# Kernel tuning notes

Measured on AMD Instinct MI355X. Metric: run time of the kernel, lower is better.

The kernel has to match this reference:

```python
import jax, jax.numpy as jnp
import numpy as np

N_U = 100000   # user nodes
N_V = 100000   # item nodes
D = 64         # input_dim
O = 64         # output_dim
R = 5          # num_support (rating levels)
E = 500000     # edges per relation


def setup_inputs() -> dict:
    key = jax.random.key(0)
    ks = jax.random.split(key, 8)
    init_range = np.sqrt(6.0 / (D + O))
    return {
        "x_u": jax.random.normal(ks[0], (N_U, D), jnp.float32),
        "x_v": jax.random.normal(ks[1], (N_V, D), jnp.float32),
        "weights_u": jax.random.uniform(ks[2], (R, D, O), jnp.float32, -init_range, init_range),
        "weights_v": jax.random.uniform(ks[3], (R, D, O), jnp.float32, -init_range, init_range),
        "bias_u": jnp.full((O,), 0.01, jnp.float32),
        "bias_v": jnp.full((O,), 0.01, jnp.float32),
        "edge_val": jax.random.uniform(ks[4], (R, E), jnp.float32),
        "edge_u": jax.random.randint(ks[5], (R, E), 0, N_U, jnp.int32),
        "edge_v": jax.random.randint(ks[6], (R, E), 0, N_V, jnp.int32),
    }


def reference(x_u, x_v, weights_u, weights_v, bias_u, bias_v, edge_val, edge_u, edge_v):
    # Cumulative (ordinal mixture) weights: wu_i = sum_{j<=i} W_u[j]
    Wu = jnp.cumsum(weights_u, axis=0)          # [R, D, O]
    Wv = jnp.cumsum(weights_v, axis=0)          # [R, D, O]

    tmp_u = jnp.einsum("nd,rdo->rno", x_u, Wu)  # [R, N_U, O]
    tmp_v = jnp.einsum("md,rdo->rmo", x_v, Wv)  # [R, N_V, O]

    gather = jax.vmap(lambda t, idx: t[idx])    # per-relation row gather

    # z_u = sum_r support_r @ tmp_v_r : scatter edge messages into user rows
    msg_u = (edge_val[..., None] * gather(tmp_v, edge_v)).reshape(R * E, O)
    z_u = jax.ops.segment_sum(msg_u, edge_u.reshape(-1), num_segments=N_U)

    # z_v = sum_r support_r^T @ tmp_u_r : scatter into item rows
    msg_v = (edge_val[..., None] * gather(tmp_u, edge_u)).reshape(R * E, O)
    z_v = jax.ops.segment_sum(msg_v, edge_v.reshape(-1), num_segments=N_V)

    u_out = jax.nn.relu(z_u + bias_u)
    v_out = jax.nn.relu(z_v + bias_v)
    return (u_out, v_out)
```

## Files before the change

kernel.cpp:

```cpp
#include <hip/hip_runtime.h>

#define N_U 100000
#define N_V 100000
#define OO 64
#define RR 5
#define EE 500000
#define TOT_E (RR * EE)
#define NB 782
#define CAP 4096
#define CAPU 3584
#define SCAT_BLOCKS 306
#define GEMM_BLOCKS 391

typedef short bf16x8 __attribute__((ext_vector_type(8)));
typedef float f32x4 __attribute__((ext_vector_type(4)));

__device__ __forceinline__ float bf2f(unsigned short u) {
  union { unsigned int i; float f; } x;
  x.i = ((unsigned int)u) << 16;
  return x.f;
}
__device__ __forceinline__ unsigned short f2bf(float f) {
  union { float f; unsigned int i; } x;
  x.f = f;
  unsigned int lsb = (x.i >> 16) & 1u;
  unsigned int r = x.i + 0x7fffu + lsb;
  return (unsigned short)(r >> 16);
}

__global__ void prep_weights(const float* __restrict__ wu,
                             const float* __restrict__ wv,
                             unsigned short* __restrict__ bfrag,
                             unsigned* __restrict__ gcur) {
  int side = blockIdx.x;
  if (gcur) {
    unsigned* g = gcur + side * 1024;
    for (int i = threadIdx.x; i < NB; i += 256) g[i] = (unsigned)i * CAP;
  }
  const float* w = side ? wv : wu;
  for (int idx = threadIdx.x; idx < 4096; idx += 256) {
    int d = idx >> 6, o = idx & 63;
    int c = o >> 4, n = o & 15;
    int sk = d >> 5, q = (d >> 3) & 3, jj = d & 7;
    int f = c * 2 + sk;
    int lane = q * 16 + n;
    int pos = (f * 64 + lane) * 8 + jj;
    float acc = 0.f;
    for (int r = 0; r < RR; ++r) {
      acc += w[r * 4096 + idx];
      bfrag[(side * RR + r) * 4096 + pos] = f2bf(acc);
    }
  }
}

__global__ __launch_bounds__(1024) void scatter_gemm(
    const int* __restrict__ dst, const int* __restrict__ src,
    const float* __restrict__ val, unsigned* __restrict__ gcursor,
    unsigned* __restrict__ keyP, unsigned short* __restrict__ valP,
    const float* __restrict__ X,
    const unsigned short* __restrict__ bfrag_side,
    unsigned short* __restrict__ tmp5) {
  __shared__ unsigned lds_u32[18972];
  int blk = blockIdx.x;
  int tid = threadIdx.x;
  if (blk < SCAT_BLOCKS) {
    unsigned* skey = lds_u32;
    unsigned short* sval = (unsigned short*)(lds_u32 + 8192);
    unsigned short* sbid = (unsigned short*)(lds_u32 + 12288);
    unsigned* cnt  = lds_u32 + 16384;
    unsigned* sc   = lds_u32 + 17166;
    unsigned* gbase = lds_u32 + 18190;
    for (int i = tid; i < NB; i += 1024) cnt[i] = 0u;
    __syncthreads();
    int base = blk * 8192;
    int t8 = base + tid * 8;
    bool full = (t8 < TOT_E);
    if (full) {
      int4 d0 = *(const int4*)(dst + t8);
      int4 d1 = *(const int4*)(dst + t8 + 4);
      atomicAdd(&cnt[d0.x >> 7], 1u);
      atomicAdd(&cnt[d0.y >> 7], 1u);
      atomicAdd(&cnt[d0.z >> 7], 1u);
      atomicAdd(&cnt[d0.w >> 7], 1u);
      atomicAdd(&cnt[d1.x >> 7], 1u);
      atomicAdd(&cnt[d1.y >> 7], 1u);
      atomicAdd(&cnt[d1.z >> 7], 1u);
      atomicAdd(&cnt[d1.w >> 7], 1u);
    }
    __syncthreads();
    sc[tid] = (tid < NB) ? cnt[tid] : 0u;
    __syncthreads();
    for (int off = 1; off < 1024; off <<= 1) {
      unsigned a = sc[tid];
      unsigned b = (tid >= off) ? sc[tid - off] : 0u;
      __syncthreads();
      sc[tid] = a + b;
      __syncthreads();
    }
    for (int b = tid; b < NB; b += 1024) {
      unsigned c = cnt[b];
      gbase[b] = c ? atomicAdd(&gcursor[b], c) : 0u;
      cnt[b] = sc[b] - c;
    }
    __syncthreads();
    unsigned total = sc[NB - 1];
    __syncthreads();
    for (int b = tid; b < NB; b += 1024) sc[b] = cnt[b];
    __syncthreads();
    if (full) {
      int4 d0 = *(const int4*)(dst + t8);
      int4 d1 = *(const int4*)(dst + t8 + 4);
      int4 s0 = *(const int4*)(src + t8);
      int4 s1 = *(const int4*)(src + t8 + 4);
      float4 v0 = *(const float4*)(val + t8);
      float4 v1 = *(const float4*)(val + t8 + 4);
      unsigned rb = (unsigned)(t8 / EE) * N_U;
#define PUT(dd, ss, vv)                                                     \
      {                                                                     \
        int bb = (dd) >> 7;                                                 \
        unsigned pos = atomicAdd(&sc[bb], 1u);                              \
        skey[pos] = (((unsigned)((dd) & 127)) << 19) | (rb + (unsigned)(ss)); \
        sval[pos] = f2bf(vv);                                               \
        sbid[pos] = (unsigned short)bb;                                     \
      }
      PUT(d0.x, s0.x, v0.x)
      PUT(d0.y, s0.y, v0.y)
      PUT(d0.z, s0.z, v0.z)
      PUT(d0.w, s0.w, v0.w)
      PUT(d1.x, s1.x, v1.x)
      PUT(d1.y, s1.y, v1.y)
      PUT(d1.z, s1.z, v1.z)
      PUT(d1.w, s1.w, v1.w)
#undef PUT
    }
    __syncthreads();
    for (int i = tid; i < (int)total; i += 1024) {
      unsigned b = sbid[i];
      unsigned addr = gbase[b] + ((unsigned)i - cnt[b]);
      keyP[addr] = skey[i];
      valP[addr] = sval[i];
    }
  } else {
    unsigned short* smem = (unsigned short*)lds_u32;
    for (int i = tid; i < 2560; i += 1024)
      ((bf16x8*)smem)[i] = ((const bf16x8*)bfrag_side)[i];
    __syncthreads();
    int lane = tid & 63;
    int wave = tid >> 6;
    int q = lane >> 4, m = lane & 15;
    int t = (blk - SCAT_BLOCKS) * 16 + wave;
    if (t >= N_U / 16) return;
    int r0 = t * 16;
    const float* xr = X + (size_t)(r0 + m) * 64;
    float4 p0 = *(const float4*)(xr + q * 8);
    float4 p1 = *(const float4*)(xr + q * 8 + 4);
    float4 p2 = *(const float4*)(xr + 32 + q * 8);
    float4 p3 = *(const float4*)(xr + 32 + q * 8 + 4);
    bf16x8 a0, a1;
    a0[0] = (short)f2bf(p0.x); a0[1] = (short)f2bf(p0.y);
    a0[2] = (short)f2bf(p0.z); a0[3] = (short)f2bf(p0.w);
    a0[4] = (short)f2bf(p1.x); a0[5] = (short)f2bf(p1.y);
    a0[6] = (short)f2bf(p1.z); a0[7] = (short)f2bf(p1.w);
    a1[0] = (short)f2bf(p2.x); a1[1] = (short)f2bf(p2.y);
    a1[2] = (short)f2bf(p2.z); a1[3] = (short)f2bf(p2.w);
    a1[4] = (short)f2bf(p3.x); a1[5] = (short)f2bf(p3.y);
    a1[6] = (short)f2bf(p3.z); a1[7] = (short)f2bf(p3.w);
    for (int r = 0; r < RR; ++r) {
      f32x4 acc[4];
#pragma unroll
      for (int c = 0; c < 4; ++c) {
        bf16x8 b0 = *(const bf16x8*)(smem + r * 4096 + ((c * 2 + 0) * 64 + lane) * 8);
        bf16x8 b1 = *(const bf16x8*)(smem + r * 4096 + ((c * 2 + 1) * 64 + lane) * 8);
        f32x4 a = {0.f, 0.f, 0.f, 0.f};
        a = __builtin_amdgcn_mfma_f32_16x16x32_bf16(a0, b0, a, 0, 0, 0);
        a = __builtin_amdgcn_mfma_f32_16x16x32_bf16(a1, b1, a, 0, 0, 0);
        acc[c] = a;
      }
      unsigned short* trow = tmp5 + (size_t)r * N_U * 64;
#pragma unroll
      for (int i = 0; i < 4; ++i) {
        ushort4 o;
        o.x = f2bf(acc[0][i]); o.y = f2bf(acc[1][i]);
        o.z = f2bf(acc[2][i]); o.w = f2bf(acc[3][i]);
        *(ushort4*)(trow + (size_t)(r0 + q * 4 + i) * 64 + m * 4) = o;
      }
    }
  }
}

__global__ __launch_bounds__(512, 8) void bucket_sort_agg(
    const unsigned* __restrict__ keyP, const unsigned short* __restrict__ valP,
    const unsigned* __restrict__ gcursor,
    const unsigned short* __restrict__ tmp5,
    const float* __restrict__ bias, float* __restrict__ out) {
  __shared__ unsigned okey[CAP];
  __shared__ unsigned short oval[CAP];
  __shared__ unsigned hist[128];
  __shared__ unsigned starts[129];
  __shared__ unsigned cur[128];
  int b = blockIdx.x;
  unsigned base = (unsigned)b * CAP;
  int cnt = (int)(gcursor[b] - base);
  if (cnt > CAPU) cnt = CAPU;
  for (int i = threadIdx.x; i < 128; i += 512) hist[i] = 0u;
  __syncthreads();
  for (int i = threadIdx.x; i < cnt; i += 512)
    atomicAdd(&hist[keyP[base + i] >> 19], 1u);
  __syncthreads();
  if (threadIdx.x == 0) {
    unsigned acc = 0u;
    for (int l = 0; l < 128; ++l) {
      starts[l] = acc;
      acc += (hist[l] + 3u) & ~3u;
    }
    starts[128] = acc;
  }
  __syncthreads();
  unsigned tot = starts[128];
  for (int i = threadIdx.x; i < (int)tot; i += 512) { okey[i] = 0u; oval[i] = 0; }
  for (int l = threadIdx.x; l < 128; l += 512) cur[l] = starts[l];
  __syncthreads();
  for (int i = threadIdx.x; i < cnt; i += 512) {
    unsigned k = keyP[base + i];
    unsigned pos = atomicAdd(&cur[k >> 19], 1u);
    okey[pos] = k & 0x7FFFFu;
    oval[pos] = valP[base + i];
  }
  __syncthreads();

  int lane = threadIdx.x & 63;
  int wave = threadIdx.x >> 6;
  int g16 = lane >> 4;
  int m = lane & 15;
  int nb0 = b * 128;
  int nodes = (N_U - nb0 < 128) ? (N_U - nb0) : 128;
  const unsigned short* tp = tmp5 + (m << 2);
  float bl = bias[lane];
  for (int l = wave; l < nodes; l += 8) {
    unsigned s = starts[l];
    unsigned e = starts[l + 1];
    float a0 = 0.f, a1 = 0.f, a2 = 0.f, a3 = 0.f;
    unsigned k = s;
    for (; k + 8 <= e; k += 8) {
      unsigned key0 = okey[k + g16];
      unsigned key1 = okey[k + 4 + g16];
      float v0 = bf2f(oval[k + g16]);
      float v1 = bf2f(oval[k + 4 + g16]);
      ushort4 t0 = *(const ushort4*)(tp + (size_t)key0 * 64);
      ushort4 t1 = *(const ushort4*)(tp + (size_t)key1 * 64);
      a0 += v0 * bf2f(t0.x);
      a1 += v0 * bf2f(t0.y);
      a2 += v0 * bf2f(t0.z);
      a3 += v0 * bf2f(t0.w);
      a0 += v1 * bf2f(t1.x);
      a1 += v1 * bf2f(t1.y);
      a2 += v1 * bf2f(t1.z);
      a3 += v1 * bf2f(t1.w);
    }
    if (k < e) {
      unsigned key0 = okey[k + g16];
      float v0 = bf2f(oval[k + g16]);
      ushort4 t0 = *(const ushort4*)(tp + (size_t)key0 * 64);
      a0 += v0 * bf2f(t0.x);
      a1 += v0 * bf2f(t0.y);
      a2 += v0 * bf2f(t0.z);
      a3 += v0 * bf2f(t0.w);
    }
    a0 += __shfl_xor(a0, 16); a0 += __shfl_xor(a0, 32);
    a1 += __shfl_xor(a1, 16); a1 += __shfl_xor(a1, 32);
    a2 += __shfl_xor(a2, 16); a2 += __shfl_xor(a2, 32);
    a3 += __shfl_xor(a3, 16); a3 += __shfl_xor(a3, 32);
    float r = (g16 & 2) ? ((g16 & 1) ? a3 : a2) : ((g16 & 1) ? a1 : a0);
    out[(size_t)(nb0 + l) * 64 + lane] = fmaxf(r + bl, 0.f);
  }
}

__global__ __launch_bounds__(256) void gemm_kernel(
    const float* __restrict__ X, const unsigned short* __restrict__ bfrag,
    unsigned short* __restrict__ tmp) {
  int lane = threadIdx.x & 63;
  int wave = threadIdx.x >> 6;
  int q = lane >> 4, m = lane & 15;
  bf16x8 bf[8];
#pragma unroll
  for (int f = 0; f < 8; ++f)
    bf[f] = *(const bf16x8*)(bfrag + (f * 64 + lane) * 8);
  int t = blockIdx.x * 4 + wave;
  if (t >= N_U / 16) return;
  int r0 = t * 16;
  const float* xr = X + (size_t)(r0 + m) * 64;
  float4 p0 = *(const float4*)(xr + q * 8);
  float4 p1 = *(const float4*)(xr + q * 8 + 4);
  float4 p2 = *(const float4*)(xr + 32 + q * 8);
  float4 p3 = *(const float4*)(xr + 32 + q * 8 + 4);
  bf16x8 a0, a1;
  a0[0] = (short)f2bf(p0.x); a0[1] = (short)f2bf(p0.y);
  a0[2] = (short)f2bf(p0.z); a0[3] = (short)f2bf(p0.w);
  a0[4] = (short)f2bf(p1.x); a0[5] = (short)f2bf(p1.y);
  a0[6] = (short)f2bf(p1.z); a0[7] = (short)f2bf(p1.w);
  a1[0] = (short)f2bf(p2.x); a1[1] = (short)f2bf(p2.y);
  a1[2] = (short)f2bf(p2.z); a1[3] = (short)f2bf(p2.w);
  a1[4] = (short)f2bf(p3.x); a1[5] = (short)f2bf(p3.y);
  a1[6] = (short)f2bf(p3.z); a1[7] = (short)f2bf(p3.w);
#pragma unroll
  for (int c = 0; c < 4; ++c) {
    f32x4 acc = {0.f, 0.f, 0.f, 0.f};
    acc = __builtin_amdgcn_mfma_f32_16x16x32_bf16(a0, bf[c * 2 + 0], acc, 0, 0, 0);
    acc = __builtin_amdgcn_mfma_f32_16x16x32_bf16(a1, bf[c * 2 + 1], acc, 0, 0, 0);
#pragma unroll
    for (int i = 0; i < 4; ++i)
      tmp[(size_t)(r0 + q * 4 + i) * 64 + c * 16 + m] = f2bf(acc[i]);
  }
}

__global__ __launch_bounds__(256) void scatter_kernel(
    const unsigned short* __restrict__ tmp, const float* __restrict__ edge_val,
    const int* __restrict__ dst_idx, const int* __restrict__ src_idx,
    float* __restrict__ z, int base, int cnt) {
  int e = blockIdx.x * 4 + (threadIdx.x >> 6);
  int j = threadIdx.x & 63;
  int d = dst_idx[e] - base;
  if ((unsigned)d >= (unsigned)cnt) return;
  int s = src_idx[e];
  float w = edge_val[e];
  atomicAdd(&z[(size_t)d * 64 + j], w * bf2f(tmp[(size_t)s * 64 + j]));
}

__global__ __launch_bounds__(256) void finalize_kernel(
    const float* __restrict__ z, const float* __restrict__ bias,
    float* __restrict__ out) {
  size_t i4 = ((size_t)blockIdx.x * 256 + threadIdx.x) * 4;
  float4 zz = *(const float4*)(z + i4);
  const float4 bb = *(const float4*)(bias + (i4 & 63));
  float4 o;
  o.x = fmaxf(zz.x + bb.x, 0.f);
  o.y = fmaxf(zz.y + bb.y, 0.f);
  o.z = fmaxf(zz.z + bb.z, 0.f);
  o.w = fmaxf(zz.w + bb.w, 0.f);
  *(float4*)(out + i4) = o;
}

extern "C" void kernel_launch(void* const* d_in, const int* in_sizes, int n_in,
                              void* d_out, int out_size, void* d_ws, size_t ws_size,
                              hipStream_t stream) {
  const float* x_u      = (const float*)d_in[0];
  const float* x_v      = (const float*)d_in[1];
  const float* w_u      = (const float*)d_in[2];
  const float* w_v      = (const float*)d_in[3];
  const float* bias_u   = (const float*)d_in[4];
  const float* bias_v   = (const float*)d_in[5];
  const float* edge_val = (const float*)d_in[6];
  const int*   edge_u   = (const int*)d_in[7];
  const int*   edge_v   = (const int*)d_in[8];
  float* out = (float*)d_out;
  char* ws = (char*)d_ws;

  const size_t FAST_NEED = 83763200;

  unsigned short* bfrag = (unsigned short*)ws;

  if (ws_size >= FAST_NEED) {
    unsigned short* tmp5 = (unsigned short*)(ws + 131072);
    unsigned*       gcur = (unsigned*)(ws + 64131072);
    unsigned*       keyP = (unsigned*)(ws + 64544768);
    unsigned short* valP = (unsigned short*)(ws + 77357056);

    prep_weights<<<2, 256, 0, stream>>>(w_u, w_v, bfrag, gcur);

    for (int side = 0; side < 2; ++side) {
      const float* X = side ? x_u : x_v;
      const unsigned short* frag0 = bfrag + (side ? 0 : RR * 4096);
      const int* dst = side ? edge_v : edge_u;
      const int* src = side ? edge_u : edge_v;
      const float* bias = side ? bias_v : bias_u;
      float* out_side = out + (size_t)side * N_U * OO;
      unsigned* gc = gcur + side * 1024;

      scatter_gemm<<<SCAT_BLOCKS + GEMM_BLOCKS, 1024, 0, stream>>>(
          dst, src, edge_val, gc, keyP, valP, X, frag0, tmp5);
      bucket_sort_agg<<<NB, 512, 0, stream>>>(keyP, valP, gc, tmp5, bias,
                                              out_side);
    }
    return;
  }

  prep_weights<<<2, 256, 0, stream>>>(w_u, w_v, bfrag, (unsigned*)0);

  unsigned short* tmp = (unsigned short*)(ws + 131072);
  float*          z   = (float*)(ws + 131072 + 12800000);
  const size_t fixed = 131072 + 12800000;
  size_t zbytes = ws_size > fixed ? ws_size - fixed : 0;
  long chunk = (long)(zbytes / (OO * 4));
  chunk -= chunk % 16;
  if (chunk < 16) chunk = 16;
  if (chunk > N_U) chunk = N_U;

  const int gemm_grid = (N_U / 16 + 3) / 4;
  const int scat_grid = EE / 4;

  for (int side = 0; side < 2; ++side) {
    const float* X = side ? x_u : x_v;
    const unsigned short* frag0 = bfrag + (side ? 0 : RR * 4096);
    const int* dst = side ? edge_v : edge_u;
    const int* src = side ? edge_u : edge_v;
    const float* bias = side ? bias_v : bias_u;
    float* out_side = out + (size_t)side * N_U * OO;

    for (long base = 0; base < N_U; base += chunk) {
      long cnt = N_U - base < chunk ? N_U - base : chunk;
      hipMemsetAsync(z, 0, (size_t)cnt * OO * 4, stream);
      for (int r = 0; r < RR; ++r) {
        gemm_kernel<<<gemm_grid, 256, 0, stream>>>(X, frag0 + r * 4096, tmp);
        scatter_kernel<<<scat_grid, 256, 0, stream>>>(
            tmp, edge_val + (size_t)r * EE, dst + (size_t)r * EE,
            src + (size_t)r * EE, z, (int)base, (int)cnt);
      }
      finalize_kernel<<<(int)(cnt / 16), 256, 0, stream>>>(
          z, bias, out_side + base * OO);
    }
  }
}
```

Measured before the change: 322.2 us.

## Partition both sides' edges in one launch, staging side-1 buckets in output buffer

Merges the two per-side scatter/GEMM launches so the first launch buckets the edges of both sides together with the first side's GEMM. The second side's partitioned keys and values live temporarily in the output buffer. This is consumed by the v-side aggregation before that region is overwritten. The second launch then runs only the remaining GEMM. The aim is better occupancy and fewer launches with serialized scatter phases, at the cost of a more complex buffer aliasing scheme.

```diff
diff --git a/kernel.cpp b/kernel.cpp
--- a/kernel.cpp
+++ b/kernel.cpp
@@ -53,17 +53,30 @@
   }
 }
 
-__global__ __launch_bounds__(1024) void scatter_gemm(
-    const int* __restrict__ dst, const int* __restrict__ src,
-    const float* __restrict__ val, unsigned* __restrict__ gcursor,
-    unsigned* __restrict__ keyP, unsigned short* __restrict__ valP,
+__global__ __launch_bounds__(1024) void mega(
+    const int* __restrict__ dst0, const int* __restrict__ src0,
+    const int* __restrict__ dst1, const int* __restrict__ src1,
+    const float* __restrict__ val,
+    unsigned* __restrict__ gcur0, unsigned* __restrict__ keyP0,
+    unsigned short* __restrict__ valP0,
+    unsigned* __restrict__ gcur1, unsigned* __restrict__ keyP1,
+    unsigned short* __restrict__ valP1,
     const float* __restrict__ X,
     const unsigned short* __restrict__ bfrag_side,
-    unsigned short* __restrict__ tmp5) {
+    unsigned short* __restrict__ tmp5,
+    int nS0, int nS1) {
   __shared__ unsigned lds_u32[18972];
   int blk = blockIdx.x;
   int tid = threadIdx.x;
-  if (blk < SCAT_BLOCKS) {
+  if (blk < nS0 + nS1) {
+    bool sB = (blk >= nS0);
+    const int* dst = sB ? dst1 : dst0;
+    const int* src = sB ? src1 : src0;
+    unsigned* gcursor = sB ? gcur1 : gcur0;
+    unsigned* keyP = sB ? keyP1 : keyP0;
+    unsigned short* valP = sB ? valP1 : valP0;
+    int sblk = sB ? blk - nS0 : blk;
+
     unsigned* skey = lds_u32;
     unsigned short* sval = (unsigned short*)(lds_u32 + 8192);
     unsigned short* sbid = (unsigned short*)(lds_u32 + 12288);
@@ -72,7 +85,7 @@
     unsigned* gbase = lds_u32 + 18190;
     for (int i = tid; i < NB; i += 1024) cnt[i] = 0u;
     __syncthreads();
-    int base = blk * 8192;
+    int base = sblk * 8192;
     int t8 = base + tid * 8;
     bool full = (t8 < TOT_E);
     if (full) {
@@ -148,7 +161,7 @@
     int lane = tid & 63;
     int wave = tid >> 6;
     int q = lane >> 4, m = lane & 15;
-    int t = (blk - SCAT_BLOCKS) * 16 + wave;
+    int t = (blk - nS0 - nS1) * 16 + wave;
     if (t >= N_U / 16) return;
     int r0 = t * 16;
     const float* xr = X + (size_t)(r0 + m) * 64;
@@ -360,27 +373,32 @@
   unsigned short* bfrag = (unsigned short*)ws;
 
   if (ws_size >= FAST_NEED) {
-    unsigned short* tmp5 = (unsigned short*)(ws + 131072);
-    unsigned*       gcur = (unsigned*)(ws + 64131072);
-    unsigned*       keyP = (unsigned*)(ws + 64544768);
-    unsigned short* valP = (unsigned short*)(ws + 77357056);
+    unsigned short* tmp5  = (unsigned short*)(ws + 131072);
+    unsigned*       gcur  = (unsigned*)(ws + 64131072);
+    unsigned*       keyP0 = (unsigned*)(ws + 64544768);
+    unsigned short* valP0 = (unsigned short*)(ws + 77357056);
+    unsigned*       keyP1 = (unsigned*)out;
+    unsigned short* valP1 = (unsigned short*)((char*)out + 12812288);
+    unsigned* gcur0 = gcur;
+    unsigned* gcur1 = gcur + 1024;
 
     prep_weights<<<2, 256, 0, stream>>>(w_u, w_v, bfrag, gcur);
 
-    for (int side = 0; side < 2; ++side) {
-      const float* X = side ? x_u : x_v;
-      const unsigned short* frag0 = bfrag + (side ? 0 : RR * 4096);
-      const int* dst = side ? edge_v : edge_u;
-      const int* src = side ? edge_u : edge_v;
-      const float* bias = side ? bias_v : bias_u;
-      float* out_side = out + (size_t)side * N_U * OO;
-      unsigned* gc = gcur + side * 1024;
-
-      scatter_gemm<<<SCAT_BLOCKS + GEMM_BLOCKS, 1024, 0, stream>>>(
-          dst, src, edge_val, gc, keyP, valP, X, frag0, tmp5);
-      bucket_sort_agg<<<NB, 512, 0, stream>>>(keyP, valP, gc, tmp5, bias,
-                                              out_side);
-    }
+    mega<<<SCAT_BLOCKS * 2 + GEMM_BLOCKS, 1024, 0, stream>>>(
+        edge_u, edge_v, edge_v, edge_u, edge_val,
+        gcur0, keyP0, valP0, gcur1, keyP1, valP1,
+        x_u, bfrag , tmp5, SCAT_BLOCKS, SCAT_BLOCKS);
+
+    bucket_sort_agg<<<NB, 512, 0, stream>>>(keyP1, valP1, gcur1, tmp5,
+                                            bias_v, out + (size_t)N_U * OO);
+
+    mega<<<GEMM_BLOCKS, 1024, 0, stream>>>(
+        edge_u, edge_v, edge_v, edge_u, edge_val,
+        gcur0, keyP0, valP0, gcur1, keyP1, valP1,
+        x_v, bfrag + RR * 4096 , tmp5, 0, 0);
+
+    bucket_sort_agg<<<NB, 512, 0, stream>>>(keyP0, valP0, gcur0, tmp5,
+                                            bias_u, out);
     return;
   }
 
```

After: 316.3 us. No clear change (-1.8%).
